# Kernel tuning notes

Hardware: AMD Instinct MI355X
Metric: run time of the kernel (lower is better)

## Reference

```python
import jax, jax.numpy as jnp
import numpy as np

N = 20000       # nodes
E = 640000      # edges
H = 128         # hidden_nf = input_nf = output_nf = d_model = d_inner (expand=1)
D_STATE = 64
D_CONV = 4
DT_RANK = 8     # ceil(d_model/16) = ceil(128/16)


def setup_inputs() -> dict:
    key = jax.random.key(0)
    ks = jax.random.split(key, 20)
    g = lambda k, shape, s=0.05: jax.random.normal(k, shape, jnp.float32) * s
    return {
        'h': g(ks[0], (N, H), 1.0),
        'coord': g(ks[1], (N, 3), 1.0),
        'edge_index': jax.random.randint(ks[2], (2, E), 0, N),
        # edge_mlp: Linear(2H+1,H) ReLU Linear(H,H) ReLU
        'W_e1': g(ks[3], (H, 2 * H + 1)), 'b_e1': jnp.zeros(H, jnp.float32),
        'W_e2': g(ks[4], (H, H)), 'b_e2': jnp.zeros(H, jnp.float32),
        # att_mlp: Linear(H,1) + sigmoid
        'w_att': g(ks[5], (1, H)), 'b_att': jnp.zeros(1, jnp.float32),
        # node_mlp: Linear(2H,H) ReLU Linear(H,H)
        'W_n1': g(ks[6], (H, 2 * H)), 'b_n1': jnp.zeros(H, jnp.float32),
        'W_n2': g(ks[7], (H, H)), 'b_n2': jnp.zeros(H, jnp.float32),
        # coord_mlp: Linear(H,H) ReLU Linear(H,1,bias=False) (xavier gain 0.001)
        'W_c1': g(ks[8], (H, H)), 'b_c1': jnp.zeros(H, jnp.float32),
        'W_c2': g(ks[9], (1, H), 0.001),
        # pre_norm LayerNorm
        'ln_g': jnp.ones(H, jnp.float32), 'ln_b': jnp.zeros(H, jnp.float32),
        # Mamba(d_model=H, d_state=64, d_conv=4, expand=1)
        'in_proj_w': g(ks[10], (2 * H, H)),
        'conv_w': g(ks[11], (H, D_CONV), 0.2), 'conv_b': jnp.zeros(H, jnp.float32),
        'x_proj_w': g(ks[12], (DT_RANK + 2 * D_STATE, H)),
        'dt_proj_w': g(ks[13], (H, DT_RANK)), 'dt_proj_b': jnp.full((H,), -4.0, jnp.float32),
        'A_log': jnp.log(jnp.broadcast_to(jnp.arange(1, D_STATE + 1, dtype=jnp.float32), (H, D_STATE))),
        'D_skip': jnp.ones(H, jnp.float32),
        'out_proj_w': g(ks[14], (H, H)),
    }


def _layernorm(x, g, b):
    mu = jnp.mean(x, -1, keepdims=True)
    var = jnp.mean((x - mu) ** 2, -1, keepdims=True)
    return (x - mu) / jnp.sqrt(var + 1e-5) * g + b


def _mamba(x, in_proj_w, conv_w, conv_b, x_proj_w, dt_proj_w, dt_proj_b, A_log, D_skip, out_proj_w):
    # x: [L, H] treated as batch-1 sequence
    L = x.shape[0]
    xz = x @ in_proj_w.T                       # [L, 2H]
    u, z = xz[:, :H], xz[:, H:]
    # causal depthwise conv1d, kernel D_CONV
    up = jnp.pad(u, ((D_CONV - 1, 0), (0, 0)))
    uc = conv_b + sum(up[k:k + L] * conv_w[:, k] for k in range(D_CONV))
    uc = jax.nn.silu(uc)                       # [L, H]
    x_dbl = uc @ x_proj_w.T                    # [L, dt_rank + 2*d_state]
    dt = jax.nn.softplus(x_dbl[:, :DT_RANK] @ dt_proj_w.T + dt_proj_b)  # [L, H]
    Bm = x_dbl[:, DT_RANK:DT_RANK + D_STATE]   # [L, d_state]
    Cm = x_dbl[:, DT_RANK + D_STATE:]          # [L, d_state]
    A = -jnp.exp(A_log)                        # [H, d_state]

    def step(s, inp):
        dt_t, b_t, c_t, u_t = inp
        s = jnp.exp(dt_t[:, None] * A) * s + (dt_t * u_t)[:, None] * b_t[None, :]
        y = jnp.sum(s * c_t[None, :], -1) + D_skip * u_t
        return s, y

    _, ys = jax.lax.scan(step, jnp.zeros((H, D_STATE), jnp.float32), (dt, Bm, Cm, uc))
    y = ys * jax.nn.silu(z)
    return y @ out_proj_w.T


def reference(h, coord, edge_index, W_e1, b_e1, W_e2, b_e2, w_att, b_att,
              W_n1, b_n1, W_n2, b_n2, W_c1, b_c1, W_c2, ln_g, ln_b,
              in_proj_w, conv_w, conv_b, x_proj_w, dt_proj_w, dt_proj_b,
              A_log, D_skip, out_proj_w):
    e0, e1 = edge_index[0], edge_index[1]
    # coord2radial (norm_diff=False)
    coord_diff = coord[e0] - coord[e1]                         # [E, 3]
    radial = jnp.sum(coord_diff ** 2, 1, keepdims=True)        # [E, 1]
    # edge_model: hi = x[e0], hj = x[e1]; cat([hj, hi, radial])
    x_edge = jnp.concatenate([h[e1], h[e0], radial], axis=1)   # [E, 2H+1]
    mij = jax.nn.relu(jax.nn.relu(x_edge @ W_e1.T + b_e1) @ W_e2.T + b_e2)
    att = jax.nn.sigmoid(mij @ w_att.T + b_att)
    edge_feat = mij * att
    mi = jax.ops.segment_sum(edge_feat, e0, num_segments=N)    # [N, H]
    # coord_model (segment mean over e0)
    t = jax.nn.relu(edge_feat @ W_c1.T + b_c1) @ W_c2.T        # [E, 1]
    trans = jnp.clip(coord_diff * t, -100.0, 100.0)
    s = jax.ops.segment_sum(trans, e0, num_segments=N)
    cnt = jax.ops.segment_sum(jnp.ones_like(trans), e0, num_segments=N)
    coord_new = coord + (s / jnp.maximum(cnt, 1.0)) * 1.0      # coords_weight=1
    # node_mlp + pre_norm + clamp
    hn = jnp.concatenate([mi, h], axis=-1)
    hn = jax.nn.relu(hn @ W_n1.T + b_n1) @ W_n2.T + b_n2
    hn = _layernorm(hn, ln_g, ln_b)
    hn = jnp.clip(hn, -10.0, 10.0)
    # mamba over node sequence (bi=False, dropout=0, mamba_mlp=False)
    out = _mamba(hn, in_proj_w, conv_w, conv_b, x_proj_w, dt_proj_w,
                 dt_proj_b, A_log, D_skip, out_proj_w)
    return out, coord_new
```

## Files before the change

### kernel.cpp

```cpp
#include <hip/hip_runtime.h>
#include <math.h>

#define NN 20000
#define EE 640000
#define HD 128
#define NC 160
#define CS 125

typedef unsigned short ushort_t;
typedef __attribute__((ext_vector_type(8))) short short8v;
typedef __attribute__((ext_vector_type(4))) float f32x4;

#define MFMA16(a,b,c) __builtin_amdgcn_mfma_f32_16x16x32_bf16(a,b,c,0,0,0)

__device__ __forceinline__ float sigf(float x) { return 1.0f / (1.0f + __expf(-x)); }

__device__ __forceinline__ ushort_t f2b(float x) {
    unsigned u = __builtin_bit_cast(unsigned, x);
    unsigned r = (u + 0x7FFFu + ((u >> 16) & 1u)) >> 16;
    return (ushort_t)r;
}
__device__ __forceinline__ float b2f(ushort_t u) {
    unsigned v = ((unsigned)u) << 16;
    return __builtin_bit_cast(float, v);
}
__device__ __forceinline__ void splitf(float v, ushort_t& h, ushort_t& l) {
    h = f2b(v);
    l = f2b(v - b2f(h));
}
__device__ __forceinline__ void cvt8x2(const float* p, short8v& hi, short8v& lo) {
    #pragma unroll
    for (int j = 0; j < 8; ++j) {
        float v = p[j];
        ushort_t h, l; splitf(v, h, l);
        hi[j] = (short)h; lo[j] = (short)l;
    }
}

__global__ __launch_bounds__(256) void hist_kernel(const int* __restrict__ ei,
                                                   int* __restrict__ histI)
{
    int i = blockIdx.x * 256 + threadIdx.x;
    if (i < EE) atomicAdd(&histI[ei[i]], 1);
}

__global__ __launch_bounds__(256) void prefix_kernel(const int* __restrict__ hist,
                                                     int* __restrict__ baseI)
{
    __shared__ int wsum[4];
    const int tid = threadIdx.x, lane = tid & 63, wid = tid >> 6;
    const int PER = 79;
    int i0 = tid * PER;
    int s = 0;
    for (int k = 0; k < PER; ++k) { int i = i0 + k; if (i < NN) s += hist[i]; }
    int v = s;
    #pragma unroll
    for (int off = 1; off < 64; off <<= 1) {
        int t = __shfl_up(v, off);
        if (lane >= off) v += t;
    }
    if (lane == 63) wsum[wid] = v;
    __syncthreads();
    if (tid == 0) {
        int acc = 0;
        #pragma unroll
        for (int w = 0; w < 4; ++w) { int t = wsum[w]; wsum[w] = acc; acc += t; }
    }
    __syncthreads();
    int excl = v - s + wsum[wid];
    for (int k = 0; k < PER; ++k) {
        int i = i0 + k;
        if (i < NN) { baseI[i] = excl; excl += hist[i]; }
    }
}

__global__ __launch_bounds__(256) void scatter_kernel(const int* __restrict__ ei,
                                                      const int* __restrict__ baseI,
                                                      int* __restrict__ cursor,
                                                      int* __restrict__ perm)
{
    int i = blockIdx.x * 256 + threadIdx.x;
    if (i < EE) {
        int n = ei[i];
        int p = baseI[n] + atomicAdd(&cursor[n], 1);
        perm[p] = i;
    }
}

__global__ __launch_bounds__(256) void prep_kernel(
    const float* __restrict__ We1, const float* __restrict__ We2,
    const float* __restrict__ Wc1, const float* __restrict__ Wn1,
    const float* __restrict__ Wn2, const float* __restrict__ Wip,
    const float* __restrict__ Wxp, const float* __restrict__ Wdt,
    const float* __restrict__ Wop,
    ushort_t* __restrict__ W12b, ushort_t* __restrict__ We2b,
    ushort_t* __restrict__ Wc1b,
    ushort_t* __restrict__ Wn1hi, ushort_t* __restrict__ Wn1lo,
    ushort_t* __restrict__ Wn2hi, ushort_t* __restrict__ Wn2lo,
    ushort_t* __restrict__ Wiphi, ushort_t* __restrict__ Wiplo,
    ushort_t* __restrict__ Wxp8hi, ushort_t* __restrict__ Wxp8lo,
    ushort_t* __restrict__ Wdt2hi, ushort_t* __restrict__ Wdt2lo,
    ushort_t* __restrict__ Wophi, ushort_t* __restrict__ Woplo)
{
    int i = blockIdx.x * 256 + threadIdx.x;
    if (i < 256 * 128) {
        int j = i >> 7, k = i & 127;
        W12b[i] = f2b(We1[(j & 127) * 257 + ((j >> 7) << 7) + k]);
        ushort_t h, l;
        splitf(Wn1[i], h, l); Wn1hi[i] = h; Wn1lo[i] = l;
        splitf(Wip[i], h, l); Wiphi[i] = h; Wiplo[i] = l;
    }
    if (i < 128 * 128) {
        We2b[i] = f2b(We2[i]);
        Wc1b[i] = f2b(Wc1[i]);
        ushort_t h, l;
        splitf(Wn2[i], h, l); Wn2hi[i] = h; Wn2lo[i] = l;
        splitf(Wop[i], h, l); Wophi[i] = h; Woplo[i] = l;
        int j = i >> 7, k = i & 127;
        splitf(Wxp[(8 + j) * 128 + k], h, l); Wxp8hi[i] = h; Wxp8lo[i] = l;
        float s = 0.f;
        #pragma unroll
        for (int r = 0; r < 8; ++r) s = fmaf(Wdt[j * 8 + r], Wxp[r * 128 + k], s);
        splitf(s, h, l); Wdt2hi[i] = h; Wdt2lo[i] = l;
    }
}

__global__ __launch_bounds__(256) void p12_kernel(
    const float* __restrict__ h, const ushort_t* __restrict__ W12b,
    ushort_t* __restrict__ P12b)
{
    const int tid = threadIdx.x;
    const int lane = tid & 63;
    const int wid = tid >> 6;
    const int wm = wid >> 1, wn = wid & 1;
    const int g = lane >> 4, r16 = lane & 15;
    const int rbase = blockIdx.x * 128 + wm * 64;

    f32x4 acc[4][8];
    #pragma unroll
    for (int mt = 0; mt < 4; ++mt)
        #pragma unroll
        for (int nt = 0; nt < 8; ++nt) acc[mt][nt] = (f32x4){0.f, 0.f, 0.f, 0.f};

    for (int c = 0; c < 4; ++c) {
        short8v afr[4], bfr[8];
        #pragma unroll
        for (int mt = 0; mt < 4; ++mt) {
            int row = rbase + mt * 16 + r16;
            if (row > NN - 1) row = NN - 1;
            const float* p = h + (size_t)row * HD + c * 32 + g * 8;
            #pragma unroll
            for (int j = 0; j < 8; ++j) afr[mt][j] = (short)f2b(p[j]);
        }
        #pragma unroll
        for (int nt = 0; nt < 8; ++nt)
            bfr[nt] = *(const short8v*)(W12b + (size_t)(wn * 128 + nt * 16 + r16) * 128 + c * 32 + g * 8);
        #pragma unroll
        for (int mt = 0; mt < 4; ++mt)
            #pragma unroll
            for (int nt = 0; nt < 8; ++nt)
                acc[mt][nt] = MFMA16(afr[mt], bfr[nt], acc[mt][nt]);
    }
    #pragma unroll
    for (int mt = 0; mt < 4; ++mt)
        #pragma unroll
        for (int nt = 0; nt < 8; ++nt)
            #pragma unroll
            for (int r = 0; r < 4; ++r) {
                int row = rbase + mt * 16 + g * 4 + r;
                if (row < NN)
                    P12b[(size_t)row * 256 + wn * 128 + nt * 16 + r16] = f2b(acc[mt][nt][r]);
            }
}

__global__ __launch_bounds__(256) void edge_mfma(
    const ushort_t* __restrict__ P12b, const float* __restrict__ coord,
    const int* __restrict__ ei, const int* __restrict__ perm,
    const float* __restrict__ We1, const float* __restrict__ be1,
    const ushort_t* __restrict__ We2b, const float* __restrict__ be2,
    const float* __restrict__ watt, const float* __restrict__ batt,
    const ushort_t* __restrict__ Wc1b, const float* __restrict__ bc1,
    const float* __restrict__ Wc2,
    float* __restrict__ mi, float* __restrict__ ssum)
{
    __shared__ ushort_t ybuf[128 * 128];
    __shared__ float rad[128];
    __shared__ float cdp[128][3];
    __shared__ float wcols[128], be1s[128], be2s[128], bc1s[128], watts[128], wc2s[128];
    __shared__ float pq[2][128];
    __shared__ int ej0s[128], ej1s[128];

    const int tid = threadIdx.x;
    const int ebase = blockIdx.x * 128;
    const int lane = tid & 63;
    const int wid = tid >> 6;
    const int wm = wid >> 1, wn = wid & 1;
    const int g = lane >> 4, r16 = lane & 15;
    const float batt0 = batt[0];

    if (tid < 128) {
        int eg = perm[ebase + tid];
        ej0s[tid] = ei[eg];
    } else {
        int t = tid - 128;
        int eg = perm[ebase + t];
        ej1s[t] = ei[EE + eg];
        wcols[t] = We1[t * 257 + 256];
        be1s[t] = be1[t]; be2s[t] = be2[t]; bc1s[t] = bc1[t];
        watts[t] = watt[t]; wc2s[t] = Wc2[t];
    }
    __syncthreads();

    short8v b2_[4][4];
    {
        const ushort_t* W2p = We2b + (size_t)(wn * 64 + r16) * 128 + g * 8;
        #pragma unroll
        for (int nt = 0; nt < 4; ++nt)
            #pragma unroll
            for (int c = 0; c < 4; ++c)
                b2_[nt][c] = *(const short8v*)(W2p + nt * 2048 + c * 32);
    }

    if (tid < 128) {
        int a = ej0s[tid], b = ej1s[tid];
        float rr = 0.f;
        #pragma unroll
        for (int c = 0; c < 3; ++c) {
            float d = coord[a * 3 + c] - coord[b * 3 + c];
            cdp[tid][c] = d; rr += d * d;
        }
        rad[tid] = rr;
    }
    __syncthreads();

    {
        const int e = tid >> 1, hf = tid & 1;
        const int n1 = ej1s[e], n0 = ej0s[e];
        const ushort_t* p1 = P12b + (size_t)n1 * 256 + hf * 64;
        const ushort_t* p2 = P12b + (size_t)n0 * 256 + 128 + hf * 64;
        const float radv = rad[e];
        const int colbase = hf * 64;
        #pragma unroll
        for (int q = 0; q < 8; ++q) {
            short8v a = *(const short8v*)(p1 + q * 8);
            short8v b = *(const short8v*)(p2 + q * 8);
            short8v ov;
            #pragma unroll
            for (int jj = 0; jj < 8; ++jj) {
                int col = colbase + q * 8 + jj;
                float v = b2f((ushort_t)a[jj]) + b2f((ushort_t)b[jj]) + radv * wcols[col] + be1s[col];
                ov[jj] = (short)f2b(fmaxf(v, 0.f));
            }
            int off = (e << 8) + ((colbase * 2 + q * 16) ^ ((e & 15) << 4));
            *(short8v*)((char*)ybuf + off) = ov;
        }
    }
    __syncthreads();

    f32x4 acc[4][4];
    #pragma unroll
    for (int mt = 0; mt < 4; ++mt)
        #pragma unroll
        for (int nt = 0; nt < 4; ++nt) acc[mt][nt] = (f32x4){0.f, 0.f, 0.f, 0.f};
    #pragma unroll
    for (int c = 0; c < 4; ++c) {
        short8v afr[4];
        #pragma unroll
        for (int mt = 0; mt < 4; ++mt) {
            int row = wm * 64 + mt * 16 + r16;
            afr[mt] = *(const short8v*)((const char*)ybuf + (row << 8) + ((c * 64 + g * 16) ^ (r16 << 4)));
        }
        #pragma unroll
        for (int mt = 0; mt < 4; ++mt)
            #pragma unroll
            for (int nt = 0; nt < 4; ++nt)
                acc[mt][nt] = MFMA16(afr[mt], b2_[nt][c], acc[mt][nt]);
    }

    short8v b3_[4][4];
    {
        const ushort_t* W3p = Wc1b + (size_t)(wn * 64 + r16) * 128 + g * 8;
        #pragma unroll
        for (int nt = 0; nt < 4; ++nt)
            #pragma unroll
            for (int c = 0; c < 4; ++c)
                b3_[nt][c] = *(const short8v*)(W3p + nt * 2048 + c * 32);
    }

    {
        float p[4][4];
        #pragma unroll
        for (int mt = 0; mt < 4; ++mt)
            #pragma unroll
            for (int r = 0; r < 4; ++r) p[mt][r] = 0.f;
        #pragma unroll
        for (int mt = 0; mt < 4; ++mt)
            #pragma unroll
            for (int nt = 0; nt < 4; ++nt)
                #pragma unroll
                for (int r = 0; r < 4; ++r) {
                    int col = wn * 64 + nt * 16 + r16;
                    float v = fmaxf(acc[mt][nt][r] + be2s[col], 0.f);
                    acc[mt][nt][r] = v;
                    p[mt][r] += v * watts[col];
                }
        #pragma unroll
        for (int off = 1; off < 16; off <<= 1)
            #pragma unroll
            for (int mt = 0; mt < 4; ++mt)
                #pragma unroll
                for (int r = 0; r < 4; ++r) p[mt][r] += __shfl_xor(p[mt][r], off);
        if (r16 == 0) {
            #pragma unroll
            for (int mt = 0; mt < 4; ++mt)
                #pragma unroll
                for (int r = 0; r < 4; ++r)
                    pq[wn][wm * 64 + mt * 16 + g * 4 + r] = p[mt][r];
        }
        __syncthreads();
        float att[4][4];
        #pragma unroll
        for (int mt = 0; mt < 4; ++mt)
            #pragma unroll
            for (int r = 0; r < 4; ++r) {
                int row = wm * 64 + mt * 16 + g * 4 + r;
                att[mt][r] = sigf(pq[0][row] + pq[1][row] + batt0);
            }
        __syncthreads();
        #pragma unroll
        for (int mt = 0; mt < 4; ++mt)
            #pragma unroll
            for (int nt = 0; nt < 4; ++nt)
                #pragma unroll
                for (int r = 0; r < 4; ++r) {
                    int row = wm * 64 + mt * 16 + g * 4 + r;
                    int col = wn * 64 + nt * 16 + r16;
                    int off = (row << 8) + (((col << 1)) ^ ((row & 15) << 4));
                    *(ushort_t*)((char*)ybuf + off) = f2b(acc[mt][nt][r] * att[mt][r]);
                }
    }
    __syncthreads();

    {
        const int col = tid & 127, half = tid >> 7;
        const int r0 = half * 64, r1 = r0 + 64;
        float sacc = 0.f; int cur = ej0s[r0];
        for (int r = r0; r < r1; ++r) {
            int node = ej0s[r];
            if (node != cur) {
                atomicAdd(&mi[(size_t)cur * HD + col], sacc);
                sacc = 0.f; cur = node;
            }
            int off = (r << 8) + (((col << 1)) ^ ((r & 15) << 4));
            sacc += b2f(*(const ushort_t*)((const char*)ybuf + off));
        }
        atomicAdd(&mi[(size_t)cur * HD + col], sacc);
    }

    #pragma unroll
    for (int mt = 0; mt < 4; ++mt)
        #pragma unroll
        for (int nt = 0; nt < 4; ++nt) acc[mt][nt] = (f32x4){0.f, 0.f, 0.f, 0.f};
    #pragma unroll
    for (int c = 0; c < 4; ++c) {
        short8v afr[4];
        #pragma unroll
        for (int mt = 0; mt < 4; ++mt) {
            int row = wm * 64 + mt * 16 + r16;
            afr[mt] = *(const short8v*)((const char*)ybuf + (row << 8) + ((c * 64 + g * 16) ^ (r16 << 4)));
        }
        #pragma unroll
        for (int mt = 0; mt < 4; ++mt)
            #pragma unroll
            for (int nt = 0; nt < 4; ++nt)
                acc[mt][nt] = MFMA16(afr[mt], b3_[nt][c], acc[mt][nt]);
    }
    {
        float q[4][4];
        #pragma unroll
        for (int mt = 0; mt < 4; ++mt)
            #pragma unroll
            for (int r = 0; r < 4; ++r) q[mt][r] = 0.f;
        #pragma unroll
        for (int mt = 0; mt < 4; ++mt)
            #pragma unroll
            for (int nt = 0; nt < 4; ++nt)
                #pragma unroll
                for (int r = 0; r < 4; ++r) {
                    int col = wn * 64 + nt * 16 + r16;
                    float v = fmaxf(acc[mt][nt][r] + bc1s[col], 0.f);
                    q[mt][r] += v * wc2s[col];
                }
        #pragma unroll
        for (int off = 1; off < 16; off <<= 1)
            #pragma unroll
            for (int mt = 0; mt < 4; ++mt)
                #pragma unroll
                for (int r = 0; r < 4; ++r) q[mt][r] += __shfl_xor(q[mt][r], off);
        if (r16 == 0) {
            #pragma unroll
            for (int mt = 0; mt < 4; ++mt)
                #pragma unroll
                for (int r = 0; r < 4; ++r)
                    pq[wn][wm * 64 + mt * 16 + g * 4 + r] = q[mt][r];
        }
        __syncthreads();
        if (tid < 6) {
            int c = tid % 3, half = tid / 3;
            int r0 = half * 64, r1 = r0 + 64;
            float sacc = 0.f; int cur = ej0s[r0];
            for (int r = r0; r < r1; ++r) {
                int node = ej0s[r];
                if (node != cur) {
                    atomicAdd(&ssum[cur * 3 + c], sacc);
                    sacc = 0.f; cur = node;
                }
                float tv = pq[0][r] + pq[1][r];
                float tr = cdp[r][c] * tv;
                tr = fminf(fmaxf(tr, -100.f), 100.f);
                sacc += tr;
            }
            atomicAdd(&ssum[cur * 3 + c], sacc);
        }
    }
}

__global__ __launch_bounds__(256) void node_mfma(
    const float* __restrict__ mi, const float* __restrict__ h,
    const ushort_t* __restrict__ Wn1hi, const ushort_t* __restrict__ Wn1lo,
    const float* __restrict__ bn1,
    const ushort_t* __restrict__ Wn2hi, const ushort_t* __restrict__ Wn2lo,
    const float* __restrict__ bn2,
    const float* __restrict__ lng, const float* __restrict__ lnb,
    float* __restrict__ hnf)
{
    __shared__ ushort_t yhi[128 * 128];
    __shared__ ushort_t ylo[128 * 128];
    __shared__ float bn1s[128], bn2s[128], lngs[128], lnbs[128];

    const int tid = threadIdx.x;
    const int nbase = blockIdx.x * 128;
    const int lane = tid & 63;
    const int wid = tid >> 6;
    const int wm = wid >> 1, wn = wid & 1;
    const int g = lane >> 4, r16 = lane & 15;

    if (tid < 128) { bn1s[tid] = bn1[tid]; bn2s[tid] = bn2[tid]; lngs[tid] = lng[tid]; lnbs[tid] = lnb[tid]; }
    __syncthreads();

    f32x4 acc[4][4];
    #pragma unroll
    for (int mt = 0; mt < 4; ++mt)
        #pragma unroll
        for (int nt = 0; nt < 4; ++nt) acc[mt][nt] = (f32x4){0.f, 0.f, 0.f, 0.f};
    for (int c = 0; c < 8; ++c) {
        short8v ahi[4], alo[4], bhi[4], blo[4];
        #pragma unroll
        for (int mt = 0; mt < 4; ++mt) {
            int row = nbase + wm * 64 + mt * 16 + r16;
            if (row > NN - 1) row = NN - 1;
            const float* src = (c < 4) ? (mi + (size_t)row * HD + c * 32 + g * 8)
                                       : (h + (size_t)row * HD + (c - 4) * 32 + g * 8);
            cvt8x2(src, ahi[mt], alo[mt]);
        }
        #pragma unroll
        for (int nt = 0; nt < 4; ++nt) {
            size_t wo = (size_t)(wn * 64 + nt * 16 + r16) * 256 + c * 32 + g * 8;
            bhi[nt] = *(const short8v*)(Wn1hi + wo);
            blo[nt] = *(const short8v*)(Wn1lo + wo);
        }
        #pragma unroll
        for (int mt = 0; mt < 4; ++mt)
            #pragma unroll
            for (int nt = 0; nt < 4; ++nt) {
                acc[mt][nt] = MFMA16(ahi[mt], bhi[nt], acc[mt][nt]);
                acc[mt][nt] = MFMA16(ahi[mt], blo[nt], acc[mt][nt]);
                acc[mt][nt] = MFMA16(alo[mt], bhi[nt], acc[mt][nt]);
            }
    }
    #pragma unroll
    for (int mt = 0; mt < 4; ++mt)
        #pragma unroll
        for (int nt = 0; nt < 4; ++nt)
            #pragma unroll
            for (int r = 0; r < 4; ++r) {
                int row = wm * 64 + mt * 16 + g * 4 + r;
                int col = wn * 64 + nt * 16 + r16;
                int off = (row << 8) + (((col << 1)) ^ ((row & 15) << 4));
                float v = fmaxf(acc[mt][nt][r] + bn1s[col], 0.f);
                ushort_t hh, ll; splitf(v, hh, ll);
                *(ushort_t*)((char*)yhi + off) = hh;
                *(ushort_t*)((char*)ylo + off) = ll;
            }
    __syncthreads();

    #pragma unroll
    for (int mt = 0; mt < 4; ++mt)
        #pragma unroll
        for (int nt = 0; nt < 4; ++nt) acc[mt][nt] = (f32x4){0.f, 0.f, 0.f, 0.f};
    #pragma unroll
    for (int c = 0; c < 4; ++c) {
        short8v ahi[4], alo[4], bhi[4], blo[4];
        #pragma unroll
        for (int mt = 0; mt < 4; ++mt) {
            int row = wm * 64 + mt * 16 + r16;
            int off = (row << 8) + ((c * 64 + g * 16) ^ (r16 << 4));
            ahi[mt] = *(const short8v*)((const char*)yhi + off);
            alo[mt] = *(const short8v*)((const char*)ylo + off);
        }
        #pragma unroll
        for (int nt = 0; nt < 4; ++nt) {
            size_t wo = (size_t)(wn * 64 + nt * 16 + r16) * 128 + c * 32 + g * 8;
            bhi[nt] = *(const short8v*)(Wn2hi + wo);
            blo[nt] = *(const short8v*)(Wn2lo + wo);
        }
        #pragma unroll
        for (int mt = 0; mt < 4; ++mt)
            #pragma unroll
            for (int nt = 0; nt < 4; ++nt) {
                acc[mt][nt] = MFMA16(ahi[mt], bhi[nt], acc[mt][nt]);
                acc[mt][nt] = MFMA16(ahi[mt], blo[nt], acc[mt][nt]);
                acc[mt][nt] = MFMA16(alo[mt], bhi[nt], acc[mt][nt]);
            }
    }
    __syncthreads();
    #pragma unroll
    for (int mt = 0; mt < 4; ++mt)
        #pragma unroll
        for (int nt = 0; nt < 4; ++nt)
            #pragma unroll
            for (int r = 0; r < 4; ++r) {
                int row = wm * 64 + mt * 16 + g * 4 + r;
                int col = wn * 64 + nt * 16 + r16;
                int off = (row << 8) + (((col << 1)) ^ ((row & 15) << 4));
                float v = acc[mt][nt][r] + bn2s[col];
                ushort_t hh, ll; splitf(v, hh, ll);
                *(ushort_t*)((char*)yhi + off) = hh;
                *(ushort_t*)((char*)ylo + off) = ll;
            }
    __syncthreads();

    {
        const int row = tid >> 1, hf = tid & 1;
        const int rowg = nbase + row;
        float s1 = 0.f, s2 = 0.f;
        float vals[64];
        #pragma unroll
        for (int q = 0; q < 8; ++q) {
            int c8 = hf * 8 + q;
            int off = (row << 8) + ((c8 * 16) ^ ((row & 15) << 4));
            short8v vh = *(const short8v*)((const char*)yhi + off);
            short8v vl = *(const short8v*)((const char*)ylo + off);
            #pragma unroll
            for (int j = 0; j < 8; ++j) {
                float v = b2f((ushort_t)vh[j]) + b2f((ushort_t)vl[j]);
                vals[q * 8 + j] = v;
                s1 += v; s2 += v * v;
            }
        }
        s1 += __shfl_xor(s1, 1);
        s2 += __shfl_xor(s2, 1);
        float mu = s1 * (1.f / HD);
        float var = s2 * (1.f / HD) - mu * mu;
        float rs = rsqrtf(fmaxf(var, 0.f) + 1e-5f);
        if (rowg < NN) {
            #pragma unroll
            for (int q = 0; q < 8; ++q) {
                int c8 = hf * 8 + q;
                f32x4 o0, o1;
                #pragma unroll
                for (int j = 0; j < 8; ++j) {
                    int col = c8 * 8 + j;
                    float v = (vals[q * 8 + j] - mu) * rs * lngs[col] + lnbs[col];
                    v = fminf(fmaxf(v, -10.f), 10.f);
                    if (j < 4) o0[j] = v; else o1[j - 4] = v;
                }
                *(f32x4*)(hnf + (size_t)rowg * HD + c8 * 8) = o0;
                *(f32x4*)(hnf + (size_t)rowg * HD + c8 * 8 + 4) = o1;
            }
        }
    }
}

__global__ __launch_bounds__(256) void coord_kernel(
    const float* __restrict__ coord, const float* __restrict__ ssum,
    const int* __restrict__ histI, float* __restrict__ outp)
{
    int idx = blockIdx.x * 256 + threadIdx.x;
    if (idx < NN * 3) {
        int n = idx / 3;
        float c = (float)histI[n];
        outp[idx] = coord[idx] + ssum[idx] / fmaxf(c, 1.f);
    }
}

__global__ __launch_bounds__(256) void xz_mfma(
    const float* __restrict__ hnf,
    const ushort_t* __restrict__ Wiphi, const ushort_t* __restrict__ Wiplo,
    ushort_t* __restrict__ ub, float* __restrict__ zs)
{
    const int tid = threadIdx.x;
    const int lane = tid & 63;
    const int wn = tid >> 6;
    const int g = lane >> 4, r16 = lane & 15;
    const int rbase = blockIdx.x * 64;

    f32x4 acc[4][4];
    #pragma unroll
    for (int mt = 0; mt < 4; ++mt)
        #pragma unroll
        for (int nt = 0; nt < 4; ++nt) acc[mt][nt] = (f32x4){0.f, 0.f, 0.f, 0.f};

    for (int c = 0; c < 4; ++c) {
        short8v ahi[4], alo[4], bhi[4], blo[4];
        #pragma unroll
        for (int mt = 0; mt < 4; ++mt) {
            int row = rbase + mt * 16 + r16;
            if (row > NN - 1) row = NN - 1;
            cvt8x2(hnf + (size_t)row * HD + c * 32 + g * 8, ahi[mt], alo[mt]);
        }
        #pragma unroll
        for (int nt = 0; nt < 4; ++nt) {
            size_t wo = (size_t)(wn * 64 + nt * 16 + r16) * 128 + c * 32 + g * 8;
            bhi[nt] = *(const short8v*)(Wiphi + wo);
            blo[nt] = *(const short8v*)(Wiplo + wo);
        }
        #pragma unroll
        for (int mt = 0; mt < 4; ++mt)
            #pragma unroll
            for (int nt = 0; nt < 4; ++nt) {
                acc[mt][nt] = MFMA16(ahi[mt], bhi[nt], acc[mt][nt]);
                acc[mt][nt] = MFMA16(ahi[mt], blo[nt], acc[mt][nt]);
                acc[mt][nt] = MFMA16(alo[mt], bhi[nt], acc[mt][nt]);
            }
    }
    #pragma unroll
    for (int mt = 0; mt < 4; ++mt)
        #pragma unroll
        for (int nt = 0; nt < 4; ++nt)
            #pragma unroll
            for (int r = 0; r < 4; ++r) {
                int row = rbase + mt * 16 + g * 4 + r;
                if (row >= NN) continue;
                int j = wn * 64 + nt * 16 + r16;
                float v = acc[mt][nt][r];
                if (j < HD) ub[(size_t)row * HD + j] = f2b(v);
                else        zs[(size_t)row * HD + (j - HD)] = v * sigf(v);
            }
}

__global__ __launch_bounds__(256) void convdt_mfma(
    const ushort_t* __restrict__ ub, const float* __restrict__ cw,
    const float* __restrict__ cb,
    const ushort_t* __restrict__ Wxp8hi, const ushort_t* __restrict__ Wxp8lo,
    const ushort_t* __restrict__ Wdt2hi, const ushort_t* __restrict__ Wdt2lo,
    const float* __restrict__ bdt,
    float* __restrict__ uc, float* __restrict__ Bm, float* __restrict__ Cm,
    float* __restrict__ dt)
{
    __shared__ ushort_t yhi[128 * 128];
    __shared__ ushort_t ylo[128 * 128];
    __shared__ float cws[128][4], cbs[128], bdts[128];

    const int tid = threadIdx.x;
    const int nbase = blockIdx.x * 128;
    const int lane = tid & 63;
    const int wid = tid >> 6;
    const int wm = wid >> 1, wn = wid & 1;
    const int g = lane >> 4, r16 = lane & 15;

    if (tid < 128) {
        cbs[tid] = cb[tid]; bdts[tid] = bdt[tid];
        #pragma unroll
        for (int k = 0; k < 4; ++k) cws[tid][k] = cw[tid * 4 + k];
    }
    __syncthreads();

    for (int it = tid; it < 128 * 16; it += 256) {
        int r = it >> 4, cg = it & 15;
        int t = nbase + r;
        int colb = cg * 8;
        float a[8];
        #pragma unroll
        for (int j = 0; j < 8; ++j) a[j] = cbs[colb + j];
        #pragma unroll
        for (int k = 0; k < 4; ++k) {
            int tt = t - 3 + k;
            if (tt >= 0 && tt < NN) {
                short8v uv = *(const short8v*)(ub + (size_t)tt * HD + colb);
                #pragma unroll
                for (int j = 0; j < 8; ++j) a[j] = fmaf(b2f((ushort_t)uv[j]), cws[colb + j][k], a[j]);
            }
        }
        short8v oh, ol;
        f32x4 u0, u1;
        #pragma unroll
        for (int j = 0; j < 8; ++j) {
            float s = (t < NN) ? a[j] * sigf(a[j]) : 0.f;
            ushort_t hh, ll; splitf(s, hh, ll);
            oh[j] = (short)hh; ol[j] = (short)ll;
            if (j < 4) u0[j] = s; else u1[j - 4] = s;
        }
        int off = (r << 8) + ((cg * 16) ^ ((r & 15) << 4));
        *(short8v*)((char*)yhi + off) = oh;
        *(short8v*)((char*)ylo + off) = ol;
        if (t < NN) {
            *(f32x4*)(uc + (size_t)t * HD + colb) = u0;
            *(f32x4*)(uc + (size_t)t * HD + colb + 4) = u1;
        }
    }
    __syncthreads();

    f32x4 acc[4][4];
    #pragma unroll
    for (int mt = 0; mt < 4; ++mt)
        #pragma unroll
        for (int nt = 0; nt < 4; ++nt) acc[mt][nt] = (f32x4){0.f, 0.f, 0.f, 0.f};
    #pragma unroll
    for (int c = 0; c < 4; ++c) {
        short8v ahi[4], alo[4], bhi[4], blo[4];
        #pragma unroll
        for (int mt = 0; mt < 4; ++mt) {
            int row = wm * 64 + mt * 16 + r16;
            int off = (row << 8) + ((c * 64 + g * 16) ^ (r16 << 4));
            ahi[mt] = *(const short8v*)((const char*)yhi + off);
            alo[mt] = *(const short8v*)((const char*)ylo + off);
        }
        #pragma unroll
        for (int nt = 0; nt < 4; ++nt) {
            size_t wo = (size_t)(wn * 64 + nt * 16 + r16) * 128 + c * 32 + g * 8;
            bhi[nt] = *(const short8v*)(Wxp8hi + wo);
            blo[nt] = *(const short8v*)(Wxp8lo + wo);
        }
        #pragma unroll
        for (int mt = 0; mt < 4; ++mt)
            #pragma unroll
            for (int nt = 0; nt < 4; ++nt) {
                acc[mt][nt] = MFMA16(ahi[mt], bhi[nt], acc[mt][nt]);
                acc[mt][nt] = MFMA16(ahi[mt], blo[nt], acc[mt][nt]);
                acc[mt][nt] = MFMA16(alo[mt], bhi[nt], acc[mt][nt]);
            }
    }
    #pragma unroll
    for (int mt = 0; mt < 4; ++mt)
        #pragma unroll
        for (int nt = 0; nt < 4; ++nt)
            #pragma unroll
            for (int r = 0; r < 4; ++r) {
                int row = nbase + wm * 64 + mt * 16 + g * 4 + r;
                if (row >= NN) continue;
                int j = wn * 64 + nt * 16 + r16;
                float v = acc[mt][nt][r];
                if (j < 64) Bm[(size_t)row * 64 + j] = v;
                else        Cm[(size_t)row * 64 + (j - 64)] = v;
            }

    #pragma unroll
    for (int mt = 0; mt < 4; ++mt)
        #pragma unroll
        for (int nt = 0; nt < 4; ++nt) acc[mt][nt] = (f32x4){0.f, 0.f, 0.f, 0.f};
    #pragma unroll
    for (int c = 0; c < 4; ++c) {
        short8v ahi[4], alo[4], bhi[4], blo[4];
        #pragma unroll
        for (int mt = 0; mt < 4; ++mt) {
            int row = wm * 64 + mt * 16 + r16;
            int off = (row << 8) + ((c * 64 + g * 16) ^ (r16 << 4));
            ahi[mt] = *(const short8v*)((const char*)yhi + off);
            alo[mt] = *(const short8v*)((const char*)ylo + off);
        }
        #pragma unroll
        for (int nt = 0; nt < 4; ++nt) {
            size_t wo = (size_t)(wn * 64 + nt * 16 + r16) * 128 + c * 32 + g * 8;
            bhi[nt] = *(const short8v*)(Wdt2hi + wo);
            blo[nt] = *(const short8v*)(Wdt2lo + wo);
        }
        #pragma unroll
        for (int mt = 0; mt < 4; ++mt)
            #pragma unroll
            for (int nt = 0; nt < 4; ++nt) {
                acc[mt][nt] = MFMA16(ahi[mt], bhi[nt], acc[mt][nt]);
                acc[mt][nt] = MFMA16(ahi[mt], blo[nt], acc[mt][nt]);
                acc[mt][nt] = MFMA16(alo[mt], bhi[nt], acc[mt][nt]);
            }
    }
    #pragma unroll
    for (int mt = 0; mt < 4; ++mt)
        #pragma unroll
        for (int nt = 0; nt < 4; ++nt)
            #pragma unroll
            for (int r = 0; r < 4; ++r) {
                int row = nbase + wm * 64 + mt * 16 + g * 4 + r;
                if (row >= NN) continue;
                int j = wn * 64 + nt * 16 + r16;
                float a = acc[mt][nt][r] + bdts[j];
                float sp = (a > 20.f) ? a : log1pf(__expf(a));
                dt[(size_t)row * HD + j] = sp;
            }
}

__global__ __launch_bounds__(256) void scan1_kernel(
    const float* __restrict__ dt, const float* __restrict__ uc,
    const float* __restrict__ Bm, const float* __restrict__ Alog,
    float* __restrict__ cP, float* __restrict__ cS)
{
    int g = blockIdx.x * 256 + threadIdx.x;
    int c = g >> 13;
    int r = g & 8191;
    int hh = r >> 6;
    int d = r & 63;
    float A = -__expf(Alog[hh * 64 + d]);
    float P = 1.f, S = 0.f;
    int t0 = c * CS;
    for (int t = t0; t < t0 + CS; ++t) {
        float dtv = dt[t * HD + hh];
        float a = __expf(dtv * A);
        float bv = Bm[t * 64 + d];
        float uv = uc[t * HD + hh];
        P *= a;
        S = fmaf(a, S, dtv * uv * bv);
    }
    cP[g] = P; cS[g] = S;
}

__global__ __launch_bounds__(256) void scan2_kernel(
    const float* __restrict__ cP, const float* __restrict__ cS, float* __restrict__ cI)
{
    int g = blockIdx.x * 256 + threadIdx.x;
    float S = 0.f;
    for (int c = 0; c < NC; ++c) {
        cI[c * 8192 + g] = S;
        S = fmaf(cP[c * 8192 + g], S, cS[c * 8192 + g]);
    }
}

__global__ __launch_bounds__(256) void scan3_kernel(
    const float* __restrict__ dt, const float* __restrict__ uc,
    const float* __restrict__ Bm, const float* __restrict__ Cm,
    const float* __restrict__ Alog, const float* __restrict__ Dskip,
    const float* __restrict__ cI, float* __restrict__ y)
{
    int g = blockIdx.x * 256 + threadIdx.x;
    int c = g >> 13;
    int r = g & 8191;
    int hh = r >> 6;
    int d = r & 63;
    float A = -__expf(Alog[hh * 64 + d]);
    float s = cI[g];
    float Dh = Dskip[hh];
    int t0 = c * CS;
    for (int t = t0; t < t0 + CS; ++t) {
        float dtv = dt[t * HD + hh];
        float a = __expf(dtv * A);
        float uv = uc[t * HD + hh];
        s = fmaf(a, s, dtv * uv * Bm[t * 64 + d]);
        float yp = s * Cm[t * 64 + d];
        #pragma unroll
        for (int off = 1; off < 64; off <<= 1) yp += __shfl_xor(yp, off);
        if (d == 0) y[t * HD + hh] = yp + Dh * uv;
    }
}

__global__ __launch_bounds__(256) void out_mfma(
    const float* __restrict__ y, const float* __restrict__ zs,
    const ushort_t* __restrict__ Wophi, const ushort_t* __restrict__ Woplo,
    float* __restrict__ outp)
{
    const int tid = threadIdx.x;
    const int lane = tid & 63;
    const int wid = tid >> 6;
    const int wm = wid >> 1, wn = wid & 1;
    const int g = lane >> 4, r16 = lane & 15;
    const int nbase = blockIdx.x * 128;

    f32x4 acc[4][4];
    #pragma unroll
    for (int mt = 0; mt < 4; ++mt)
        #pragma unroll
        for (int nt = 0; nt < 4; ++nt) acc[mt][nt] = (f32x4){0.f, 0.f, 0.f, 0.f};

    for (int c = 0; c < 4; ++c) {
        short8v ahi[4], alo[4], bhi[4], blo[4];
        #pragma unroll
        for (int mt = 0; mt < 4; ++mt) {
            int row = nbase + wm * 64 + mt * 16 + r16;
            if (row > NN - 1) row = NN - 1;
            const float* yp = y + (size_t)row * HD + c * 32 + g * 8;
            const float* zp = zs + (size_t)row * HD + c * 32 + g * 8;
            #pragma unroll
            for (int j = 0; j < 8; ++j) {
                float v = yp[j] * zp[j];
                ushort_t hh, ll; splitf(v, hh, ll);
                ahi[mt][j] = (short)hh; alo[mt][j] = (short)ll;
            }
        }
        #pragma unroll
        for (int nt = 0; nt < 4; ++nt) {
            size_t wo = (size_t)(wn * 64 + nt * 16 + r16) * 128 + c * 32 + g * 8;
            bhi[nt] = *(const short8v*)(Wophi + wo);
            blo[nt] = *(const short8v*)(Woplo + wo);
        }
        #pragma unroll
        for (int mt = 0; mt < 4; ++mt)
            #pragma unroll
            for (int nt = 0; nt < 4; ++nt) {
                acc[mt][nt] = MFMA16(ahi[mt], bhi[nt], acc[mt][nt]);
                acc[mt][nt] = MFMA16(ahi[mt], blo[nt], acc[mt][nt]);
                acc[mt][nt] = MFMA16(alo[mt], bhi[nt], acc[mt][nt]);
            }
    }
    #pragma unroll
    for (int mt = 0; mt < 4; ++mt)
        #pragma unroll
        for (int nt = 0; nt < 4; ++nt)
            #pragma unroll
            for (int r = 0; r < 4; ++r) {
                int row = nbase + wm * 64 + mt * 16 + g * 4 + r;
                if (row < NN)
                    outp[(size_t)row * HD + wn * 64 + nt * 16 + r16] = acc[mt][nt][r];
            }
}

extern "C" void kernel_launch(void* const* d_in, const int* in_sizes, int n_in,
                              void* d_out, int out_size, void* d_ws, size_t ws_size,
                              hipStream_t stream)
{
    const float* h     = (const float*)d_in[0];
    const float* coord = (const float*)d_in[1];
    const int*   ei    = (const int*)d_in[2];
    const float* We1   = (const float*)d_in[3];
    const float* be1   = (const float*)d_in[4];
    const float* We2   = (const float*)d_in[5];
    const float* be2   = (const float*)d_in[6];
    const float* watt  = (const float*)d_in[7];
    const float* batt  = (const float*)d_in[8];
    const float* Wn1   = (const float*)d_in[9];
    const float* bn1   = (const float*)d_in[10];
    const float* Wn2   = (const float*)d_in[11];
    const float* bn2   = (const float*)d_in[12];
    const float* Wc1   = (const float*)d_in[13];
    const float* bc1   = (const float*)d_in[14];
    const float* Wc2   = (const float*)d_in[15];
    const float* lng   = (const float*)d_in[16];
    const float* lnb   = (const float*)d_in[17];
    const float* Wip   = (const float*)d_in[18];
    const float* convw = (const float*)d_in[19];
    const float* convb = (const float*)d_in[20];
    const float* Wxp   = (const float*)d_in[21];
    const float* Wdt   = (const float*)d_in[22];
    const float* bdt   = (const float*)d_in[23];
    const float* Alog  = (const float*)d_in[24];
    const float* Dskip = (const float*)d_in[25];
    const float* Wop   = (const float*)d_in[26];

    float* ws   = (float*)d_ws;
    float* mi   = ws;
    float* ssum = mi   + (size_t)NN * HD;
    int*   histI  = (int*)(ssum + (size_t)NN * 3);
    int*   cursor = histI + NN;
    int*   baseI  = cursor + NN;
    int*   perm   = baseI + NN;
    float* zsb  = (float*)(perm + EE);
    float* ucb  = zsb  + (size_t)NN * HD;
    float* dtb  = ucb  + (size_t)NN * HD;
    float* Bm   = dtb  + (size_t)NN * HD;
    float* Cm   = Bm   + (size_t)NN * 64;
    float* cP   = Cm   + (size_t)NN * 64;
    float* cSb  = cP   + (size_t)NC * 8192;
    float* cIb  = cSb  + (size_t)NC * 8192;
    ushort_t* ub    = (ushort_t*)(cIb + (size_t)NC * 8192);
    ushort_t* W12bp = ub + (size_t)NN * HD;
    ushort_t* We2bp = W12bp + 256 * 128;
    ushort_t* Wc1bp = We2bp + 128 * 128;
    ushort_t* Wn1hi = Wc1bp + 128 * 128;
    ushort_t* Wn1lo = Wn1hi + 128 * 256;
    ushort_t* Wn2hi = Wn1lo + 128 * 256;
    ushort_t* Wn2lo = Wn2hi + 128 * 128;
    ushort_t* Wiphi = Wn2lo + 128 * 128;
    ushort_t* Wiplo = Wiphi + 256 * 128;
    ushort_t* Wxp8hi = Wiplo + 256 * 128;
    ushort_t* Wxp8lo = Wxp8hi + 128 * 128;
    ushort_t* Wdt2hi = Wxp8lo + 128 * 128;
    ushort_t* Wdt2lo = Wdt2hi + 128 * 128;
    ushort_t* Wophi  = Wdt2lo + 128 * 128;
    ushort_t* Woplo  = Wophi + 128 * 128;
    ushort_t* P12bp = (ushort_t*)cP;
    float* hnf = cP;
    float* yb = mi;

    float* outp     = (float*)d_out;
    float* coordout = outp + (size_t)NN * HD;

    hipMemsetAsync(ws, 0, (size_t)NN * 133 * 4, stream);

    hist_kernel<<<(EE + 255) / 256, 256, 0, stream>>>(ei, histI);
    prefix_kernel<<<1, 256, 0, stream>>>(histI, baseI);
    scatter_kernel<<<(EE + 255) / 256, 256, 0, stream>>>(ei, baseI, cursor, perm);
    prep_kernel<<<128, 256, 0, stream>>>(We1, We2, Wc1, Wn1, Wn2, Wip, Wxp, Wdt, Wop,
                                         W12bp, We2bp, Wc1bp,
                                         Wn1hi, Wn1lo, Wn2hi, Wn2lo, Wiphi, Wiplo,
                                         Wxp8hi, Wxp8lo, Wdt2hi, Wdt2lo, Wophi, Woplo);
    p12_kernel<<<(NN + 127) / 128, 256, 0, stream>>>(h, W12bp, P12bp);
    edge_mfma<<<EE / 128, 256, 0, stream>>>(P12bp, coord, ei, perm, We1, be1,
                                            We2bp, be2, watt, batt, Wc1bp, bc1, Wc2,
                                            mi, ssum);
    node_mfma<<<(NN + 127) / 128, 256, 0, stream>>>(mi, h, Wn1hi, Wn1lo, bn1,
                                                    Wn2hi, Wn2lo, bn2, lng, lnb, hnf);
    coord_kernel<<<(NN * 3 + 255) / 256, 256, 0, stream>>>(coord, ssum, histI, coordout);
    xz_mfma<<<(NN + 63) / 64, 256, 0, stream>>>(hnf, Wiphi, Wiplo, ub, zsb);
    convdt_mfma<<<(NN + 127) / 128, 256, 0, stream>>>(ub, convw, convb,
                                                      Wxp8hi, Wxp8lo, Wdt2hi, Wdt2lo,
                                                      bdt, ucb, Bm, Cm, dtb);
    scan1_kernel<<<NC * 8192 / 256, 256, 0, stream>>>(dtb, ucb, Bm, Alog, cP, cSb);
    scan2_kernel<<<8192 / 256, 256, 0, stream>>>(cP, cSb, cIb);
    scan3_kernel<<<NC * 8192 / 256, 256, 0, stream>>>(dtb, ucb, Bm, Cm, Alog, Dskip, cIb, yb);
    out_mfma<<<(NN + 127) / 128, 256, 0, stream>>>(yb, zsb, Wophi, Woplo, outp);
}
```

Before: 795.7 us.

## Restructure edge gather, segment reductions, prefix scan width, and scan3 state packing

The edge kernel now has each thread load its own edge indices and gather P12 rows into registers before the first barrier. This removes one syncthreads and the shared rad/ej1s staging, and lets the gather overlap with the bias loads. The Wc1 fragment load moves later to ease register pressure. The mi segment reduction uses vectorized 8-wide rows over 16-row segments, and the coord reduction uses 48 threads instead of 6. The prefix kernel now runs 1024 threads, and scan3 handles two states per thread with 32-lane shuffles. The trade-off is more atomics from the shorter segments and higher register use for the gathered data.

Measured after the change: 773.9 us. 2.7% less time.

```diff
diff --git a/kernel.cpp b/kernel.cpp
--- a/kernel.cpp
+++ b/kernel.cpp
@@ -44,12 +44,12 @@
     if (i < EE) atomicAdd(&histI[ei[i]], 1);
 }
 
-__global__ __launch_bounds__(256) void prefix_kernel(const int* __restrict__ hist,
-                                                     int* __restrict__ baseI)
-{
-    __shared__ int wsum[4];
+__global__ __launch_bounds__(1024) void prefix_kernel(const int* __restrict__ hist,
+                                                      int* __restrict__ baseI)
+{
+    __shared__ int wsum[16];
     const int tid = threadIdx.x, lane = tid & 63, wid = tid >> 6;
-    const int PER = 79;
+    const int PER = 20;
     int i0 = tid * PER;
     int s = 0;
     for (int k = 0; k < PER; ++k) { int i = i0 + k; if (i < NN) s += hist[i]; }
@@ -64,7 +64,7 @@
     if (tid == 0) {
         int acc = 0;
         #pragma unroll
-        for (int w = 0; w < 4; ++w) { int t = wsum[w]; wsum[w] = acc; acc += t; }
+        for (int w = 0; w < 16; ++w) { int t = wsum[w]; wsum[w] = acc; acc += t; }
     }
     __syncthreads();
     int excl = v - s + wsum[wid];
@@ -184,11 +184,10 @@
     float* __restrict__ mi, float* __restrict__ ssum)
 {
     __shared__ ushort_t ybuf[128 * 128];
-    __shared__ float rad[128];
     __shared__ float cdp[128][3];
     __shared__ float wcols[128], be1s[128], be2s[128], bc1s[128], watts[128], wc2s[128];
     __shared__ float pq[2][128];
-    __shared__ int ej0s[128], ej1s[128];
+    __shared__ int ej0s[128];
 
     const int tid = threadIdx.x;
     const int ebase = blockIdx.x * 128;
@@ -198,19 +197,58 @@
     const int g = lane >> 4, r16 = lane & 15;
     const float batt0 = batt[0];
 
-    if (tid < 128) {
-        int eg = perm[ebase + tid];
-        ej0s[tid] = ei[eg];
-    } else {
-        int t = tid - 128;
-        int eg = perm[ebase + t];
-        ej1s[t] = ei[EE + eg];
-        wcols[t] = We1[t * 257 + 256];
-        be1s[t] = be1[t]; be2s[t] = be2[t]; bc1s[t] = bc1[t];
-        watts[t] = watt[t]; wc2s[t] = Wc2[t];
+    const int e = tid >> 1, hf = tid & 1;
+    const int eg = perm[ebase + e];
+    const int n0 = ei[eg];
+    const int n1 = ei[EE + eg];
+    short8v ga[8], gb[8];
+    {
+        const ushort_t* p1 = P12b + (size_t)n1 * 256 + hf * 64;
+        const ushort_t* p2 = P12b + (size_t)n0 * 256 + 128 + hf * 64;
+        #pragma unroll
+        for (int q = 0; q < 8; ++q) {
+            ga[q] = *(const short8v*)(p1 + q * 8);
+            gb[q] = *(const short8v*)(p2 + q * 8);
+        }
+    }
+    if (hf == 0) ej0s[e] = n0;
+    {
+        int t = tid & 127;
+        if (tid < 128) {
+            wcols[t] = We1[t * 257 + 256];
+            be1s[t] = be1[t];
+            be2s[t] = be2[t];
+        } else {
+            bc1s[t] = bc1[t];
+            watts[t] = watt[t];
+            wc2s[t] = Wc2[t];
+        }
+    }
+    float rr;
+    {
+        float d0 = coord[n0 * 3 + 0] - coord[n1 * 3 + 0];
+        float d1 = coord[n0 * 3 + 1] - coord[n1 * 3 + 1];
+        float d2 = coord[n0 * 3 + 2] - coord[n1 * 3 + 2];
+        rr = d0 * d0 + d1 * d1 + d2 * d2;
+        if (hf == 0) { cdp[e][0] = d0; cdp[e][1] = d1; cdp[e][2] = d2; }
     }
     __syncthreads();
 
+    {
+        const int colbase = hf * 64;
+        #pragma unroll
+        for (int q = 0; q < 8; ++q) {
+            short8v ov;
+            #pragma unroll
+            for (int jj = 0; jj < 8; ++jj) {
+                int col = colbase + q * 8 + jj;
+                float v = b2f((ushort_t)ga[q][jj]) + b2f((ushort_t)gb[q][jj]) + rr * wcols[col] + be1s[col];
+                ov[jj] = (short)f2b(fmaxf(v, 0.f));
+            }
+            int off = (e << 8) + ((colbase * 2 + q * 16) ^ ((e & 15) << 4));
+            *(short8v*)((char*)ybuf + off) = ov;
+        }
+    }
     short8v b2_[4][4];
     {
         const ushort_t* W2p = We2b + (size_t)(wn * 64 + r16) * 128 + g * 8;
@@ -220,41 +258,6 @@
             for (int c = 0; c < 4; ++c)
                 b2_[nt][c] = *(const short8v*)(W2p + nt * 2048 + c * 32);
     }
-
-    if (tid < 128) {
-        int a = ej0s[tid], b = ej1s[tid];
-        float rr = 0.f;
-        #pragma unroll
-        for (int c = 0; c < 3; ++c) {
-            float d = coord[a * 3 + c] - coord[b * 3 + c];
-            cdp[tid][c] = d; rr += d * d;
-        }
-        rad[tid] = rr;
-    }
-    __syncthreads();
-
-    {
-        const int e = tid >> 1, hf = tid & 1;
-        const int n1 = ej1s[e], n0 = ej0s[e];
-        const ushort_t* p1 = P12b + (size_t)n1 * 256 + hf * 64;
-        const ushort_t* p2 = P12b + (size_t)n0 * 256 + 128 + hf * 64;
-        const float radv = rad[e];
-        const int colbase = hf * 64;
-        #pragma unroll
-        for (int q = 0; q < 8; ++q) {
-            short8v a = *(const short8v*)(p1 + q * 8);
-            short8v b = *(const short8v*)(p2 + q * 8);
-            short8v ov;
-            #pragma unroll
-            for (int jj = 0; jj < 8; ++jj) {
-                int col = colbase + q * 8 + jj;
-                float v = b2f((ushort_t)a[jj]) + b2f((ushort_t)b[jj]) + radv * wcols[col] + be1s[col];
-                ov[jj] = (short)f2b(fmaxf(v, 0.f));
-            }
-            int off = (e << 8) + ((colbase * 2 + q * 16) ^ ((e & 15) << 4));
-            *(short8v*)((char*)ybuf + off) = ov;
-        }
-    }
     __syncthreads();
 
     f32x4 acc[4][4];
@@ -275,16 +278,6 @@
             #pragma unroll
             for (int nt = 0; nt < 4; ++nt)
                 acc[mt][nt] = MFMA16(afr[mt], b2_[nt][c], acc[mt][nt]);
-    }
-
-    short8v b3_[4][4];
-    {
-        const ushort_t* W3p = Wc1b + (size_t)(wn * 64 + r16) * 128 + g * 8;
-        #pragma unroll
-        for (int nt = 0; nt < 4; ++nt)
-            #pragma unroll
-            for (int c = 0; c < 4; ++c)
-                b3_[nt][c] = *(const short8v*)(W3p + nt * 2048 + c * 32);
     }
 
     {
@@ -341,20 +334,40 @@
     }
     __syncthreads();
 
+    short8v b3_[4][4];
     {
-        const int col = tid & 127, half = tid >> 7;
-        const int r0 = half * 64, r1 = r0 + 64;
-        float sacc = 0.f; int cur = ej0s[r0];
-        for (int r = r0; r < r1; ++r) {
+        const ushort_t* W3p = Wc1b + (size_t)(wn * 64 + r16) * 128 + g * 8;
+        #pragma unroll
+        for (int nt = 0; nt < 4; ++nt)
+            #pragma unroll
+            for (int c = 0; c < 4; ++c)
+                b3_[nt][c] = *(const short8v*)(W3p + nt * 2048 + c * 32);
+    }
+
+    if (tid < 128) {
+        const int cg = tid & 15;
+        const int rg = tid >> 4;
+        const int r0 = rg * 16;
+        float sa[8];
+        #pragma unroll
+        for (int j = 0; j < 8; ++j) sa[j] = 0.f;
+        int cur = ej0s[r0];
+        for (int r = r0; r < r0 + 16; ++r) {
             int node = ej0s[r];
             if (node != cur) {
-                atomicAdd(&mi[(size_t)cur * HD + col], sacc);
-                sacc = 0.f; cur = node;
-            }
-            int off = (r << 8) + (((col << 1)) ^ ((r & 15) << 4));
-            sacc += b2f(*(const ushort_t*)((const char*)ybuf + off));
-        }
-        atomicAdd(&mi[(size_t)cur * HD + col], sacc);
+                #pragma unroll
+                for (int j = 0; j < 8; ++j) atomicAdd(&mi[(size_t)cur * HD + cg * 8 + j], sa[j]);
+                #pragma unroll
+                for (int j = 0; j < 8; ++j) sa[j] = 0.f;
+                cur = node;
+            }
+            int off = (r << 8) + ((cg * 16) ^ ((r & 15) << 4));
+            short8v v = *(const short8v*)((const char*)ybuf + off);
+            #pragma unroll
+            for (int j = 0; j < 8; ++j) sa[j] += b2f((ushort_t)v[j]);
+        }
+        #pragma unroll
+        for (int j = 0; j < 8; ++j) atomicAdd(&mi[(size_t)cur * HD + cg * 8 + j], sa[j]);
     }
 
     #pragma unroll
@@ -405,9 +418,9 @@
                     pq[wn][wm * 64 + mt * 16 + g * 4 + r] = q[mt][r];
         }
         __syncthreads();
-        if (tid < 6) {
-            int c = tid % 3, half = tid / 3;
-            int r0 = half * 64, r1 = r0 + 64;
+        if (tid < 48) {
+            int c = tid % 3, seg = tid / 3;
+            int r0 = seg * 8, r1 = r0 + 8;
             float sacc = 0.f; int cur = ej0s[r0];
             for (int r = r0; r < r1; ++r) {
                 int node = ej0s[r];
@@ -841,23 +854,29 @@
     const float* __restrict__ cI, float* __restrict__ y)
 {
     int g = blockIdx.x * 256 + threadIdx.x;
-    int c = g >> 13;
-    int r = g & 8191;
-    int hh = r >> 6;
-    int d = r & 63;
-    float A = -__expf(Alog[hh * 64 + d]);
-    float s = cI[g];
+    int c = g >> 12;
+    int r = g & 4095;
+    int hh = r >> 5;
+    int dp = (r & 31) * 2;
+    float A0 = -__expf(Alog[hh * 64 + dp]);
+    float A1 = -__expf(Alog[hh * 64 + dp + 1]);
+    float s0 = cI[c * 8192 + hh * 64 + dp];
+    float s1 = cI[c * 8192 + hh * 64 + dp + 1];
     float Dh = Dskip[hh];
     int t0 = c * CS;
+    const int lane31 = threadIdx.x & 31;
     for (int t = t0; t < t0 + CS; ++t) {
         float dtv = dt[t * HD + hh];
-        float a = __expf(dtv * A);
         float uv = uc[t * HD + hh];
-        s = fmaf(a, s, dtv * uv * Bm[t * 64 + d]);
-        float yp = s * Cm[t * 64 + d];
-        #pragma unroll
-        for (int off = 1; off < 64; off <<= 1) yp += __shfl_xor(yp, off);
-        if (d == 0) y[t * HD + hh] = yp + Dh * uv;
+        float du = dtv * uv;
+        float2 bv = *(const float2*)(Bm + (size_t)t * 64 + dp);
+        float2 cv = *(const float2*)(Cm + (size_t)t * 64 + dp);
+        s0 = fmaf(__expf(dtv * A0), s0, du * bv.x);
+        s1 = fmaf(__expf(dtv * A1), s1, du * bv.y);
+        float yp = fmaf(s0, cv.x, s1 * cv.y);
+        #pragma unroll
+        for (int off = 1; off < 32; off <<= 1) yp += __shfl_xor(yp, off);
+        if (lane31 == 0) y[t * HD + hh] = yp + Dh * uv;
     }
 }
 
@@ -994,7 +1013,7 @@
     hipMemsetAsync(ws, 0, (size_t)NN * 133 * 4, stream);
 
     hist_kernel<<<(EE + 255) / 256, 256, 0, stream>>>(ei, histI);
-    prefix_kernel<<<1, 256, 0, stream>>>(histI, baseI);
+    prefix_kernel<<<1, 1024, 0, stream>>>(histI, baseI);
     scatter_kernel<<<(EE + 255) / 256, 256, 0, stream>>>(ei, baseI, cursor, perm);
     prep_kernel<<<128, 256, 0, stream>>>(We1, We2, Wc1, Wn1, Wn2, Wip, Wxp, Wdt, Wop,
                                          W12bp, We2bp, Wc1bp,
@@ -1013,6 +1032,6 @@
                                                       bdt, ucb, Bm, Cm, dtb);
     scan1_kernel<<<NC * 8192 / 256, 256, 0, stream>>>(dtb, ucb, Bm, Alog, cP, cSb);
     scan2_kernel<<<8192 / 256, 256, 0, stream>>>(cP, cSb, cIb);
-    scan3_kernel<<<NC * 8192 / 256, 256, 0, stream>>>(dtb, ucb, Bm, Cm, Alog, Dskip, cIb, yb);
+    scan3_kernel<<<NC * 4096 / 256, 256, 0, stream>>>(dtb, ucb, Bm, Cm, Alog, Dskip, cIb, yb);
     out_mfma<<<(NN + 127) / 128, 256, 0, stream>>>(yb, zsb, Wophi, Woplo, outp);
 }
```
